# Optimization experiments

Hardware: AMD Instinct MI355X
Metric: run time of the kernel (lower is better)

Reference implementation:

```python
import jax, jax.numpy as jnp
import numpy as np

WS = 8      # window size
SS = 4      # shift size
NH = 4      # num heads
EPS = 1e-5
MLP_RATIO = 4


def _win_part(x, ws):
    # x: [B,D,H,W,C] -> [B*nD*nH*nW, ws^3, C]
    B, D, H, W, C = x.shape
    x = x.reshape(B, D // ws, ws, H // ws, ws, W // ws, ws, C)
    x = x.transpose(0, 1, 3, 5, 2, 4, 6, 7)
    return x.reshape(-1, ws * ws * ws, C)


def _win_rev(w, ws, B, D, H, W):
    C = w.shape[-1]
    x = w.reshape(B, D // ws, H // ws, W // ws, ws, ws, ws, C)
    x = x.transpose(0, 1, 4, 2, 5, 3, 6, 7)
    return x.reshape(B, D, H, W, C)


def _ln(x, g, b):
    m = jnp.mean(x, axis=-1, keepdims=True)
    v = jnp.mean((x - m) ** 2, axis=-1, keepdims=True)
    return (x - m) / jnp.sqrt(v + EPS) * g + b


def _rel_index(ws):
    coords = np.stack(np.meshgrid(np.arange(ws), np.arange(ws), np.arange(ws), indexing='ij'))  # [3,ws,ws,ws]
    cf = coords.reshape(3, -1)                      # [3, ws^3]
    rel = (cf[:, :, None] - cf[:, None, :]).transpose(1, 2, 0) + (ws - 1)  # [N,N,3]
    return rel[..., 0] * (2 * ws - 1) ** 2 + rel[..., 1] * (2 * ws - 1) + rel[..., 2]


def _attn_mask(D, H, W, ws, ss):
    img = np.zeros((1, D, H, W, 1), dtype=np.float32)
    cnt = 0
    sl = (slice(0, -ws), slice(-ws, -ss), slice(-ss, None))
    for d in sl:
        for h in sl:
            for w in sl:
                img[:, d, h, w, :] = cnt
                cnt += 1
    mw = np.asarray(_win_part(jnp.asarray(img), ws))[..., 0]  # [nW, ws^3]
    diff = mw[:, None, :] - mw[:, :, None]
    return np.where(diff != 0, -100.0, 0.0).astype(np.float32)


def setup_inputs() -> dict:
    key = jax.random.key(0)
    ks = jax.random.split(key, 12)
    B, D, H, W, C = 1, 16, 64, 64, 128
    mh = MLP_RATIO * C
    s = 0.02
    return {
        'x': jax.random.normal(ks[0], (B, D, H, W, C), jnp.float32),
        'attn_mask': jnp.asarray(_attn_mask(D, H, W, WS, SS)),
        'rel_index': jnp.asarray(_rel_index(WS), jnp.int32),
        'rel_bias': jax.random.normal(ks[1], ((2 * WS - 1) ** 3, NH), jnp.float32) * s,
        'qkv_w': jax.random.normal(ks[2], (3 * C, C), jnp.float32) * s,
        'qkv_b': jnp.zeros((3 * C,), jnp.float32),
        'proj_w': jax.random.normal(ks[3], (C, C), jnp.float32) * s,
        'proj_b': jnp.zeros((C,), jnp.float32),
        'norm1_g': jnp.ones((C,), jnp.float32),
        'norm1_b': jnp.zeros((C,), jnp.float32),
        'norm2_g': jnp.ones((C,), jnp.float32),
        'norm2_b': jnp.zeros((C,), jnp.float32),
        'mlp_w1': jax.random.normal(ks[4], (mh, C), jnp.float32) * s,
        'mlp_b1': jnp.zeros((mh,), jnp.float32),
        'mlp_w2': jax.random.normal(ks[5], (C, mh), jnp.float32) * s,
        'mlp_b2': jnp.zeros((C,), jnp.float32),
    }


def reference(x, attn_mask, rel_index, rel_bias, qkv_w, qkv_b, proj_w, proj_b,
              norm1_g, norm1_b, norm2_g, norm2_b, mlp_w1, mlp_b1, mlp_w2, mlp_b2):
    B, D, H, W, C = x.shape
    ws, ss, nh = WS, SS, NH
    hd = C // nh
    scale = hd ** -0.5
    N = ws ** 3
    shortcut = x
    h = _ln(x, norm1_g, norm1_b)
    h = jnp.roll(h, (-ss, -ss, -ss), axis=(1, 2, 3))
    xw = _win_part(h, ws)                 # [B_, N, C]
    B_ = xw.shape[0]
    nW = attn_mask.shape[0]
    qkv = xw @ qkv_w.T + qkv_b            # [B_, N, 3C]
    qkv = qkv.reshape(B_, N, 3, nh, hd).transpose(2, 0, 3, 1, 4)  # [3,B_,h,N,hd]
    q, k, v = qkv[0] * scale, qkv[1], qkv[2]
    attn = jnp.einsum('bhnd,bhmd->bhnm', q, k)
    rpe = rel_bias[rel_index.reshape(-1)].reshape(N, N, nh).transpose(2, 0, 1)  # [h,N,N]
    attn = attn + rpe[None]
    attn = attn.reshape(B_ // nW, nW, nh, N, N) + attn_mask[None, :, None]
    attn = jax.nn.softmax(attn.reshape(B_, nh, N, N), axis=-1)
    out = jnp.einsum('bhnm,bhmd->bhnd', attn, v).transpose(0, 2, 1, 3).reshape(B_, N, C)
    out = out @ proj_w.T + proj_b
    out = _win_rev(out, ws, B, D, H, W)
    out = jnp.roll(out, (ss, ss, ss), axis=(1, 2, 3))
    x = shortcut + out
    h2 = _ln(x, norm2_g, norm2_b)
    h2 = jax.nn.gelu(h2 @ mlp_w1.T + mlp_b1, approximate=False)
    return x + h2 @ mlp_w2.T + mlp_b2
```

## Files before the change

kernel.cpp:

```cpp
#include <hip/hip_runtime.h>
#include <math.h>

typedef __bf16 bf16;
typedef __bf16 bf16x4 __attribute__((ext_vector_type(4)));
typedef __bf16 bf16x8 __attribute__((ext_vector_type(8)));
typedef float f32x4 __attribute__((ext_vector_type(4)));
typedef unsigned short u16;
typedef u16 u16x2 __attribute__((ext_vector_type(2)));

#define LOG2E 1.4426950408889634f

__device__ __forceinline__ float b2f(u16 b) {
  return (float)__builtin_bit_cast(bf16, b);
}

__global__ void sniff_k(const unsigned* __restrict__ xw_, int* __restrict__ flag) {
  int lane = threadIdx.x;
  int c = 0;
#pragma unroll
  for (int j = 0; j < 4; j++) {
    unsigned e = (xw_[lane * 4 + j] >> 7) & 0xFFu;
    c += (e >= 100u && e <= 140u) ? 1 : 0;
  }
#pragma unroll
  for (int d = 1; d < 64; d <<= 1) c += __shfl_xor(c, d);
  if (lane == 0) *flag = (c >= 150) ? 1 : 0;
}

__global__ __launch_bounds__(256) void canon_big_k(const void* __restrict__ src,
                                                   bf16* __restrict__ dst,
                                                   const int* __restrict__ flag) {
  int i = (blockIdx.x * 256 + threadIdx.x) * 8;
  if (*flag) {
    *(bf16x8*)&dst[i] = *(const bf16x8*)((const bf16*)src + i);
  } else {
    const float* s = (const float*)src + i;
    bf16x8 v;
#pragma unroll
    for (int j = 0; j < 8; j++) v[j] = (bf16)s[j];
    *(bf16x8*)&dst[i] = v;
  }
}

struct CanonArgs {
  const void* src[13];
  bf16* dst[13];
  int n[13];
};

__global__ __launch_bounds__(256) void canon_small_k(CanonArgs a,
                                                     const int* __restrict__ flag) {
  int ti = blockIdx.y;
  int i = blockIdx.x * 256 + threadIdx.x;
  if (i >= a.n[ti]) return;
  if (*flag)
    a.dst[ti][i] = ((const bf16*)a.src[ti])[i];
  else
    a.dst[ti][i] = (bf16)((const float*)a.src[ti])[i];
}

__global__ __launch_bounds__(256) void rpem_k(const int* __restrict__ ridx,
                                              const bf16* __restrict__ rbias,
                                              bf16* __restrict__ rpem) {
  int t = blockIdx.x * 256 + threadIdx.x;
  int m0 = (t & 127) * 4, q = (t >> 7) & 511, h = (t >> 16) & 3, ty = t >> 18;
  int qd = q >> 6, qh = (q >> 3) & 7, qw = q & 7;
  int4 ri = *(const int4*)&ridx[q * 512 + m0];
  const int rv[4] = {ri.x, ri.y, ri.z, ri.w};
  bf16x4 o;
#pragma unroll
  for (int j = 0; j < 4; j++) {
    int m = m0 + j;
    int md = m >> 6, mh = (m >> 3) & 7, mw = m & 7;
    bool diff = ((ty & 4) && ((qd < 4) != (md < 4))) ||
                ((ty & 2) && ((qh < 4) != (mh < 4))) ||
                ((ty & 1) && ((qw < 4) != (mw < 4)));
    float v = (float)rbias[rv[j] * 4 + h] * LOG2E;
    o[j] = (bf16)(v + (diff ? -144.2695041f : 0.f));
  }
  *(bf16x4*)&rpem[(size_t)t * 4] = o;
}

template <int ROLL>
__global__ __launch_bounds__(256) void ln_k(const bf16* __restrict__ x,
                                            const bf16* __restrict__ g,
                                            const bf16* __restrict__ bsh,
                                            bf16* __restrict__ out) {
  int wave = threadIdx.x >> 6, lane = threadIdx.x & 63;
  int tok = blockIdx.x * 4 + wave;
  size_t src;
  if (ROLL) {
    int win = tok >> 9, pos = tok & 511;
    int rd = (win >> 6) * 8 + (pos >> 6);
    int rh = ((win >> 3) & 7) * 8 + ((pos >> 3) & 7);
    int rw = (win & 7) * 8 + (pos & 7);
    int od = (rd + 4) & 15, oh = (rh + 4) & 63, ow = (rw + 4) & 63;
    src = (size_t)((od * 64 + oh) * 64 + ow) * 128;
  } else {
    src = (size_t)tok * 128;
  }
  int ch = lane * 2;
  u16x2 xv = *(const u16x2*)(x + src + ch);
  float f0 = b2f(xv[0]), f1 = b2f(xv[1]);
  float s = f0 + f1, sq = f0 * f0 + f1 * f1;
#pragma unroll
  for (int d = 1; d < 64; d <<= 1) {
    s += __shfl_xor(s, d);
    sq += __shfl_xor(sq, d);
  }
  float mean = s * (1.f / 128.f);
  float var = sq * (1.f / 128.f) - mean * mean;
  float rstd = rsqrtf(fmaxf(var, 0.f) + 1e-5f);
  u16x2 gv = *(const u16x2*)(g + ch), bv = *(const u16x2*)(bsh + ch);
  u16x2 ov;
  ov[0] = __builtin_bit_cast(u16, (bf16)((f0 - mean) * rstd * b2f(gv[0]) + b2f(bv[0])));
  ov[1] = __builtin_bit_cast(u16, (bf16)((f1 - mean) * rstd * b2f(gv[1]) + b2f(bv[1])));
  *(u16x2*)(out + (size_t)tok * 128 + ch) = ov;
}

template <int EPI, int BM, int N_, int K_>
__global__ __launch_bounds__(256) void gemm_k(const bf16* __restrict__ A,
                                              const bf16* __restrict__ B,
                                              const bf16* __restrict__ bias,
                                              void* __restrict__ outv,
                                              const bf16* __restrict__ resid,
                                              const int* __restrict__ flag) {
  __shared__ __align__(16) u16 As[BM * 72];
  __shared__ __align__(16) u16 Bs[128 * 72];
  const int t = threadIdx.x;
  const int wave = t >> 6, lane = t & 63, l15 = lane & 15, quad = lane >> 4;
  const int m0 = blockIdx.x * BM, n0 = blockIdx.y * 128;
  constexpr int MI = BM / 32;
  constexpr int PA = BM / 32;
  int fl = 0;
  if constexpr (EPI == 3) fl = *flag;
  f32x4 acc[MI][4] = {};
  const int wr = (wave >> 1) * (BM / 2), wc = (wave & 1) * 64;
  const int srow = t >> 3, scol = (t & 7) * 8;
  constexpr int NC = K_ / 64;
  bf16x8 avA[PA], avB[PA];
#pragma unroll
  for (int p = 0; p < PA; p++) {
    int row = p * 32 + srow;
    avA[p] = *(const bf16x8*)(A + (size_t)(m0 + row) * K_ + scol);
  }
#pragma unroll
  for (int c = 0; c < NC; c++) {
    const bf16x8* av = (c & 1) ? avB : avA;
    bf16x8* avN = (c & 1) ? avA : avB;
    if (c + 1 < NC) {
#pragma unroll
      for (int p = 0; p < PA; p++) {
        int row = p * 32 + srow;
        avN[p] = *(const bf16x8*)(A + (size_t)(m0 + row) * K_ + (c + 1) * 64 + scol);
      }
    }
    bf16x8 bv[4];
#pragma unroll
    for (int p = 0; p < 4; p++) {
      int row = p * 32 + srow;
      bv[p] = *(const bf16x8*)(B + (size_t)(n0 + row) * K_ + c * 64 + scol);
    }
    __syncthreads();
#pragma unroll
    for (int p = 0; p < PA; p++)
      *(bf16x8*)&As[(p * 32 + srow) * 72 + scol] = av[p];
#pragma unroll
    for (int p = 0; p < 4; p++)
      *(bf16x8*)&Bs[(p * 32 + srow) * 72 + scol] = bv[p];
    __syncthreads();
#pragma unroll
    for (int ks = 0; ks < 2; ks++) {
      bf16x8 a[MI], b[4];
#pragma unroll
      for (int i = 0; i < MI; i++)
        a[i] = *(const bf16x8*)&As[(wr + i * 16 + l15) * 72 + ks * 32 + quad * 8];
#pragma unroll
      for (int j = 0; j < 4; j++)
        b[j] = *(const bf16x8*)&Bs[(wc + j * 16 + l15) * 72 + ks * 32 + quad * 8];
#pragma unroll
      for (int i = 0; i < MI; i++)
#pragma unroll
        for (int j = 0; j < 4; j++)
          acc[i][j] =
              __builtin_amdgcn_mfma_f32_16x16x32_bf16(a[i], b[j], acc[i][j], 0, 0, 0);
    }
  }
  const float qscale = 0.17677669529663687f * LOG2E;
#pragma unroll
  for (int i = 0; i < MI; i++) {
#pragma unroll
    for (int r = 0; r < 4; r++) {
      int tok = m0 + wr + i * 16 + quad * 4 + r;
      size_t obase = 0;
      if constexpr (EPI == 1) {
        int win = tok >> 9, pos = tok & 511;
        int rd = (win >> 6) * 8 + (pos >> 6);
        int rh = ((win >> 3) & 7) * 8 + ((pos >> 3) & 7);
        int rw = (win & 7) * 8 + (pos & 7);
        int od = (rd + 4) & 15, oh = (rh + 4) & 63, ow = (rw + 4) & 63;
        obase = (size_t)((od * 64 + oh) * 64 + ow) * 128;
      } else if constexpr (EPI != 0) {
        obase = (size_t)tok * N_;
      }
#pragma unroll
      for (int j = 0; j < 4; j++) {
        int gn = n0 + wc + j * 16 + l15;
        float v = acc[i][j][r] + (float)bias[gn];
        if constexpr (EPI == 0) {
          int tensor = gn >> 7, c = gn & 127, head = c >> 5, d = c & 31;
          if (tensor == 0) v *= qscale;
          int win = tok >> 9, pos = tok & 511;
          size_t off = ((((size_t)tensor * 4 + head) * 128 + win) * 512 + pos) * 32 + d;
          ((bf16*)outv)[off] = (bf16)v;
        } else if constexpr (EPI == 1) {
          v += (float)resid[obase + gn];
          ((bf16*)outv)[obase + gn] = (bf16)v;
        } else if constexpr (EPI == 2) {
          float v2 = v * v;
          float u2 = v * (2.30220806f + 0.10294323f * v2);
          float e2 = exp2f(u2);
          float rcp = __builtin_amdgcn_rcpf(e2 + 1.f);
          v = v - v * rcp;
          ((bf16*)outv)[obase + gn] = (bf16)v;
        } else {
          v += (float)resid[obase + gn];
          if (fl)
            ((bf16*)outv)[obase + gn] = (bf16)v;
          else
            ((float*)outv)[obase + gn] = v;
        }
      }
    }
  }
}

__global__ __launch_bounds__(512) void attn_k(const bf16* __restrict__ qkv,
                                              const bf16* __restrict__ rpem,
                                              bf16* __restrict__ att) {
  __shared__ __align__(16) bf16 sVt[32 * 512];
  __shared__ __align__(16) bf16 sP[8][32 * 64];
  const int t = threadIdx.x;
  const int p = blockIdx.x;
  const int win = ((p >> 6) << 3) | (p & 7);
  const int mid = (p >> 3) & 7;
  const int head = mid >> 1, qh = mid & 1;
  const int wave = t >> 6, lane = t & 63, l15 = lane & 15, quad = lane >> 4;

  const int wd = win >> 6, wh = (win >> 3) & 7, ww = win & 7;
  const int type = ((wd == 1) << 2) | ((wh == 7) << 1) | (ww == 7);

  const size_t hw32 = (size_t)512 * 32;
  const bf16* qp = qkv + ((size_t)(0 * 4 + head) * 128 + win) * hw32;
  const bf16* kp = qkv + ((size_t)(1 * 4 + head) * 128 + win) * hw32;
  const bf16* vp = qkv + ((size_t)(2 * 4 + head) * 128 + win) * hw32;
  const bf16* rpeh = rpem + (size_t)(type * 4 + head) * 512 * 512;
  const int qbase = qh * 256 + wave * 32;

  {
    int kpi = t >> 3, dblk = (t & 7) * 4;
    char* sb = (char*)sVt;
#pragma unroll
    for (int kb = 0; kb < 4; kb++) {
      const bf16* v0 = vp + (size_t)(kb * 128 + 2 * kpi) * 32 + dblk;
      bf16x4 a = *(const bf16x4*)v0;
      bf16x4 b = *(const bf16x4*)(v0 + 32);
      int keyw = kb * 64 + kpi;
#pragma unroll
      for (int dd = 0; dd < 4; dd++) {
        int row = dblk + dd;
        unsigned wv = (unsigned)__builtin_bit_cast(u16, a[dd]) |
                      ((unsigned)__builtin_bit_cast(u16, b[dd]) << 16);
        *(unsigned*)(sb + ((row * 1024 + keyw * 4) ^ ((row & 7) << 4))) = wv;
      }
    }
  }

  bf16x8 qa[2];
#pragma unroll
  for (int nt = 0; nt < 2; nt++)
    qa[nt] = *(const bf16x8*)(qp + (size_t)(qbase + nt * 16 + l15) * 32 + quad * 8);

  bf16x8 kb[4];
  bf16x4 rv[4][2];
#pragma unroll
  for (int mt = 0; mt < 4; mt++) {
    kb[mt] = *(const bf16x8*)(kp + (size_t)(mt * 16 + l15) * 32 + quad * 8);
#pragma unroll
    for (int nt = 0; nt < 2; nt++)
      rv[mt][nt] = *(const bf16x4*)(rpeh + (size_t)(qbase + nt * 16 + l15) * 512 +
                                    mt * 16 + quad * 4);
  }

  __syncthreads();

  f32x4 O[2][2] = {};
  float ls[2] = {0.f, 0.f};
  char* pw = (char*)sP[wave];
  const char* sv = (const char*)sVt;
  const int swz = (l15 & 7) << 4;

#pragma unroll
  for (int kt = 0; kt < 8; kt++) {
    bf16x8 kbn[4];
    bf16x4 rvn[4][2];
    if (kt < 7) {
#pragma unroll
      for (int mt = 0; mt < 4; mt++) {
        kbn[mt] = *(const bf16x8*)(kp +
                                   (size_t)((kt + 1) * 64 + mt * 16 + l15) * 32 +
                                   quad * 8);
#pragma unroll
        for (int nt = 0; nt < 2; nt++)
          rvn[mt][nt] =
              *(const bf16x4*)(rpeh + (size_t)(qbase + nt * 16 + l15) * 512 +
                               (kt + 1) * 64 + mt * 16 + quad * 4);
      }
    }
    f32x4 S[4][2];
#pragma unroll
    for (int mt = 0; mt < 4; mt++)
#pragma unroll
      for (int nt = 0; nt < 2; nt++) {
        f32x4 c;
#pragma unroll
        for (int r = 0; r < 4; r++) c[r] = (float)rv[mt][nt][r];
        S[mt][nt] = __builtin_amdgcn_mfma_f32_16x16x32_bf16(kb[mt], qa[nt], c, 0, 0, 0);
      }
#pragma unroll
    for (int nt = 0; nt < 2; nt++)
#pragma unroll
      for (int mt = 0; mt < 4; mt++) {
        bf16x4 pv;
#pragma unroll
        for (int r = 0; r < 4; r++) {
          float pe = exp2f(S[mt][nt][r]);
          ls[nt] += pe;
          pv[r] = (bf16)pe;
        }
        *(bf16x4*)(pw + (((nt * 16 + l15) * 128 + mt * 32 + quad * 8) ^ swz)) = pv;
      }
#pragma unroll
    for (int s = 0; s < 2; s++) {
      int vc = kt * 128 + s * 64 + quad * 16;
      int pc = s * 64 + quad * 16;
      bf16x8 va0 = *(const bf16x8*)(sv + ((l15 * 1024 + vc) ^ swz));
      bf16x8 va1 = *(const bf16x8*)(sv + (((16 + l15) * 1024 + vc) ^ swz));
      bf16x8 pb0 = *(const bf16x8*)(pw + ((l15 * 128 + pc) ^ swz));
      bf16x8 pb1 = *(const bf16x8*)(pw + (((16 + l15) * 128 + pc) ^ swz));
      O[0][0] = __builtin_amdgcn_mfma_f32_16x16x32_bf16(va0, pb0, O[0][0], 0, 0, 0);
      O[0][1] = __builtin_amdgcn_mfma_f32_16x16x32_bf16(va0, pb1, O[0][1], 0, 0, 0);
      O[1][0] = __builtin_amdgcn_mfma_f32_16x16x32_bf16(va1, pb0, O[1][0], 0, 0, 0);
      O[1][1] = __builtin_amdgcn_mfma_f32_16x16x32_bf16(va1, pb1, O[1][1], 0, 0, 0);
    }
#pragma unroll
    for (int mt = 0; mt < 4; mt++) {
      kb[mt] = kbn[mt];
      rv[mt][0] = rvn[mt][0];
      rv[mt][1] = rvn[mt][1];
    }
  }
#pragma unroll
  for (int nt = 0; nt < 2; nt++) {
    float l = ls[nt];
    l += __shfl_xor(l, 16);
    l += __shfl_xor(l, 32);
    float inv = __builtin_amdgcn_rcpf(l);
    int q = qbase + nt * 16 + l15;
#pragma unroll
    for (int dm = 0; dm < 2; dm++) {
      bf16x4 o;
#pragma unroll
      for (int r = 0; r < 4; r++) o[r] = (bf16)(O[dm][nt][r] * inv);
      *(bf16x4*)(att + ((size_t)win * 512 + q) * 128 + head * 32 + dm * 16 +
                 quad * 4) = o;
    }
  }
}

extern "C" void kernel_launch(void* const* d_in, const int* in_sizes, int n_in,
                              void* d_out, int out_size, void* d_ws,
                              size_t ws_size, hipStream_t stream) {
  const int* rel_index = (const int*)d_in[2];
  char* w = (char*)d_ws;

  int* flag = (int*)w;
  bf16* rb_c = (bf16*)(w + (64ull << 10));
  bf16* qw_c = (bf16*)(w + (128ull << 10));
  bf16* pw_c = (bf16*)(w + (256ull << 10));
  bf16* w1_c = (bf16*)(w + (320ull << 10));
  bf16* w2_c = (bf16*)(w + (512ull << 10));
  bf16* qb_c = (bf16*)(w + (704ull << 10));
  bf16* pb_c = (bf16*)(w + (708ull << 10));
  bf16* g1_c = (bf16*)(w + (712ull << 10));
  bf16* b1n_c = (bf16*)(w + (716ull << 10));
  bf16* g2_c = (bf16*)(w + (720ull << 10));
  bf16* b2n_c = (bf16*)(w + (724ull << 10));
  bf16* mb1_c = (bf16*)(w + (728ull << 10));
  bf16* mb2_c = (bf16*)(w + (732ull << 10));
  bf16* x_c = (bf16*)(w + (1ull << 20));
  bf16* xw = (bf16*)(w + (17ull << 20));
  bf16* qkvb = (bf16*)(w + (33ull << 20));
  bf16* x2 = (bf16*)(w + (99ull << 20));
  bf16* rpem = x2;
  bf16* att = xw;
  bf16* h2 = xw;
  bf16* a1 = qkvb;

  sniff_k<<<1, 64, 0, stream>>>((const unsigned*)d_in[0], flag);
  canon_big_k<<<4096, 256, 0, stream>>>(d_in[0], x_c, flag);

  CanonArgs ca;
  const int srcidx[13] = {3, 4, 5, 6, 7, 8, 9, 10, 11, 12, 13, 14, 15};
  bf16* dsts[13] = {rb_c, qw_c, qb_c, pw_c, pb_c, g1_c, b1n_c,
                    g2_c, b2n_c, w1_c, mb1_c, w2_c, mb2_c};
  for (int i = 0; i < 13; i++) {
    ca.src[i] = d_in[srcidx[i]];
    ca.dst[i] = dsts[i];
    ca.n[i] = in_sizes[srcidx[i]];
  }
  canon_small_k<<<dim3(256, 13), 256, 0, stream>>>(ca, flag);

  rpem_k<<<8192, 256, 0, stream>>>(rel_index, rb_c, rpem);
  ln_k<1><<<16384, 256, 0, stream>>>(x_c, g1_c, b1n_c, xw);
  gemm_k<0, 128, 384, 128><<<dim3(512, 3), 256, 0, stream>>>(xw, qw_c, qb_c,
                                                             qkvb, nullptr, flag);
  attn_k<<<1024, 512, 0, stream>>>(qkvb, rpem, att);
  gemm_k<1, 64, 128, 128><<<dim3(1024, 1), 256, 0, stream>>>(att, pw_c, pb_c,
                                                             x2, x_c, flag);
  ln_k<0><<<16384, 256, 0, stream>>>(x2, g2_c, b2n_c, h2);
  gemm_k<2, 128, 512, 128><<<dim3(512, 4), 256, 0, stream>>>(h2, w1_c, mb1_c,
                                                             a1, nullptr, flag);
  gemm_k<3, 64, 128, 512><<<dim3(1024, 1), 256, 0, stream>>>(a1, w2_c, mb2_c,
                                                             d_out, x2, flag);
}
```

Baseline: 461.6 us.

## Stage GEMM epilogue through LDS for vectorized stores; restructure attention row-sum

The GEMM epilogue now writes biased and activated results into shared memory, then re-reads them row-wise so each thread issues 16-byte vectorized global stores and residual loads instead of scattered 2-byte accesses. The attention kernel drops its register double-buffering of K and bias, stops unrolling the key loop, and adds an occupancy hint (launch_bounds 512,4) to cut register pressure. It also computes the softmax denominator with an MFMA against a ones vector, replacing per-lane adds and shuffles. The cost is an extra LDS round trip and barriers in the GEMM, less load/compute overlap in attention, and extra MFMA work.

```diff
diff --git a/kernel.cpp b/kernel.cpp
--- a/kernel.cpp
+++ b/kernel.cpp
@@ -125,8 +125,9 @@
                                               void* __restrict__ outv,
                                               const bf16* __restrict__ resid,
                                               const int* __restrict__ flag) {
-  __shared__ __align__(16) u16 As[BM * 72];
-  __shared__ __align__(16) u16 Bs[128 * 72];
+  __shared__ __align__(16) u16 SMEM[BM * 72 + 128 * 72];
+  u16* As = SMEM;
+  u16* Bs = SMEM + BM * 72;
   const int t = threadIdx.x;
   const int wave = t >> 6, lane = t & 63, l15 = lane & 15, quad = lane >> 4;
   const int m0 = blockIdx.x * BM, n0 = blockIdx.y * 128;
@@ -186,58 +187,91 @@
               __builtin_amdgcn_mfma_f32_16x16x32_bf16(a[i], b[j], acc[i][j], 0, 0, 0);
     }
   }
+  __syncthreads();
+  u16* Cs = SMEM;
   const float qscale = 0.17677669529663687f * LOG2E;
 #pragma unroll
-  for (int i = 0; i < MI; i++) {
-#pragma unroll
-    for (int r = 0; r < 4; r++) {
-      int tok = m0 + wr + i * 16 + quad * 4 + r;
-      size_t obase = 0;
-      if constexpr (EPI == 1) {
-        int win = tok >> 9, pos = tok & 511;
-        int rd = (win >> 6) * 8 + (pos >> 6);
-        int rh = ((win >> 3) & 7) * 8 + ((pos >> 3) & 7);
-        int rw = (win & 7) * 8 + (pos & 7);
-        int od = (rd + 4) & 15, oh = (rh + 4) & 63, ow = (rw + 4) & 63;
-        obase = (size_t)((od * 64 + oh) * 64 + ow) * 128;
-      } else if constexpr (EPI != 0) {
-        obase = (size_t)tok * N_;
-      }
-#pragma unroll
-      for (int j = 0; j < 4; j++) {
-        int gn = n0 + wc + j * 16 + l15;
-        float v = acc[i][j][r] + (float)bias[gn];
+  for (int i = 0; i < MI; i++)
+#pragma unroll
+    for (int j = 0; j < 4; j++) {
+      int c = wc + j * 16 + l15;
+      float bj = (float)bias[n0 + c];
+#pragma unroll
+      for (int r = 0; r < 4; r++) {
+        float v = acc[i][j][r] + bj;
         if constexpr (EPI == 0) {
-          int tensor = gn >> 7, c = gn & 127, head = c >> 5, d = c & 31;
-          if (tensor == 0) v *= qscale;
-          int win = tok >> 9, pos = tok & 511;
-          size_t off = ((((size_t)tensor * 4 + head) * 128 + win) * 512 + pos) * 32 + d;
-          ((bf16*)outv)[off] = (bf16)v;
-        } else if constexpr (EPI == 1) {
-          v += (float)resid[obase + gn];
-          ((bf16*)outv)[obase + gn] = (bf16)v;
-        } else if constexpr (EPI == 2) {
+          if (n0 == 0) v *= qscale;
+        }
+        if constexpr (EPI == 2) {
           float v2 = v * v;
           float u2 = v * (2.30220806f + 0.10294323f * v2);
           float e2 = exp2f(u2);
           float rcp = __builtin_amdgcn_rcpf(e2 + 1.f);
           v = v - v * rcp;
-          ((bf16*)outv)[obase + gn] = (bf16)v;
-        } else {
-          v += (float)resid[obase + gn];
-          if (fl)
-            ((bf16*)outv)[obase + gn] = (bf16)v;
-          else
-            ((float*)outv)[obase + gn] = v;
         }
-      }
-    }
-  }
-}
-
-__global__ __launch_bounds__(512) void attn_k(const bf16* __restrict__ qkv,
-                                              const bf16* __restrict__ rpem,
-                                              bf16* __restrict__ att) {
+        Cs[(wr + i * 16 + quad * 4 + r) * 136 + c] =
+            __builtin_bit_cast(u16, (bf16)v);
+      }
+    }
+  __syncthreads();
+  constexpr int TPR = 256 / BM;
+  constexpr int CPT = 128 / TPR;
+  const int row = t / TPR, chb = (t % TPR) * CPT;
+  const int tok = m0 + row;
+  size_t obase = 0;
+  if constexpr (EPI == 1) {
+    int win = tok >> 9, pos = tok & 511;
+    int rd = (win >> 6) * 8 + (pos >> 6);
+    int rh = ((win >> 3) & 7) * 8 + ((pos >> 3) & 7);
+    int rw = (win & 7) * 8 + (pos & 7);
+    int od = (rd + 4) & 15, oh = (rh + 4) & 63, ow = (rw + 4) & 63;
+    obase = (size_t)((od * 64 + oh) * 64 + ow) * 128;
+  } else if constexpr (EPI == 2) {
+    obase = (size_t)tok * N_ + n0;
+  } else if constexpr (EPI == 3) {
+    obase = (size_t)tok * N_;
+  }
+#pragma unroll
+  for (int cc = 0; cc < CPT / 8; cc++) {
+    int c0 = chb + cc * 8;
+    bf16x8 cv = *(const bf16x8*)&Cs[row * 136 + c0];
+    if constexpr (EPI == 0) {
+      int win = tok >> 9, pos = tok & 511;
+      int tensor = n0 >> 7, head = c0 >> 5, d = c0 & 31;
+      size_t off =
+          ((((size_t)tensor * 4 + head) * 128 + win) * 512 + pos) * 32 + d;
+      *(bf16x8*)((bf16*)outv + off) = cv;
+    } else if constexpr (EPI == 1) {
+      bf16x8 rv8 = *(const bf16x8*)(resid + obase + c0);
+      bf16x8 o;
+#pragma unroll
+      for (int e = 0; e < 8; e++) o[e] = (bf16)((float)cv[e] + (float)rv8[e]);
+      *(bf16x8*)((bf16*)outv + obase + c0) = o;
+    } else if constexpr (EPI == 2) {
+      *(bf16x8*)((bf16*)outv + obase + c0) = cv;
+    } else {
+      bf16x8 rv8 = *(const bf16x8*)(resid + obase + c0);
+      float fo[8];
+#pragma unroll
+      for (int e = 0; e < 8; e++) fo[e] = (float)cv[e] + (float)rv8[e];
+      if (fl) {
+        bf16x8 o;
+#pragma unroll
+        for (int e = 0; e < 8; e++) o[e] = (bf16)fo[e];
+        *(bf16x8*)((bf16*)outv + obase + c0) = o;
+      } else {
+        f32x4 o0 = {fo[0], fo[1], fo[2], fo[3]};
+        f32x4 o1 = {fo[4], fo[5], fo[6], fo[7]};
+        *(f32x4*)((float*)outv + obase + c0) = o0;
+        *(f32x4*)((float*)outv + obase + c0 + 4) = o1;
+      }
+    }
+  }
+}
+
+__global__ __launch_bounds__(512, 4) void attn_k(const bf16* __restrict__ qkv,
+                                                 const bf16* __restrict__ rpem,
+                                                 bf16* __restrict__ att) {
   __shared__ __align__(16) bf16 sVt[32 * 512];
   __shared__ __align__(16) bf16 sP[8][32 * 64];
   const int t = threadIdx.x;
@@ -281,41 +315,31 @@
   for (int nt = 0; nt < 2; nt++)
     qa[nt] = *(const bf16x8*)(qp + (size_t)(qbase + nt * 16 + l15) * 32 + quad * 8);
 
-  bf16x8 kb[4];
-  bf16x4 rv[4][2];
-#pragma unroll
-  for (int mt = 0; mt < 4; mt++) {
-    kb[mt] = *(const bf16x8*)(kp + (size_t)(mt * 16 + l15) * 32 + quad * 8);
-#pragma unroll
-    for (int nt = 0; nt < 2; nt++)
-      rv[mt][nt] = *(const bf16x4*)(rpeh + (size_t)(qbase + nt * 16 + l15) * 512 +
-                                    mt * 16 + quad * 4);
-  }
+  bf16x8 ones;
+#pragma unroll
+  for (int e = 0; e < 8; e++) ones[e] = (bf16)1.0f;
 
   __syncthreads();
 
   f32x4 O[2][2] = {};
-  float ls[2] = {0.f, 0.f};
+  f32x4 O2[2] = {};
   char* pw = (char*)sP[wave];
   const char* sv = (const char*)sVt;
   const int swz = (l15 & 7) << 4;
 
-#pragma unroll
+#pragma unroll 1
   for (int kt = 0; kt < 8; kt++) {
-    bf16x8 kbn[4];
-    bf16x4 rvn[4][2];
-    if (kt < 7) {
-#pragma unroll
-      for (int mt = 0; mt < 4; mt++) {
-        kbn[mt] = *(const bf16x8*)(kp +
-                                   (size_t)((kt + 1) * 64 + mt * 16 + l15) * 32 +
-                                   quad * 8);
-#pragma unroll
-        for (int nt = 0; nt < 2; nt++)
-          rvn[mt][nt] =
-              *(const bf16x4*)(rpeh + (size_t)(qbase + nt * 16 + l15) * 512 +
-                               (kt + 1) * 64 + mt * 16 + quad * 4);
-      }
+    bf16x8 kb[4];
+    bf16x4 rv[4][2];
+#pragma unroll
+    for (int mt = 0; mt < 4; mt++) {
+      kb[mt] = *(const bf16x8*)(kp + (size_t)(kt * 64 + mt * 16 + l15) * 32 +
+                                quad * 8);
+#pragma unroll
+      for (int nt = 0; nt < 2; nt++)
+        rv[mt][nt] =
+            *(const bf16x4*)(rpeh + (size_t)(qbase + nt * 16 + l15) * 512 +
+                             kt * 64 + mt * 16 + quad * 4);
     }
     f32x4 S[4][2];
 #pragma unroll
@@ -333,11 +357,7 @@
       for (int mt = 0; mt < 4; mt++) {
         bf16x4 pv;
 #pragma unroll
-        for (int r = 0; r < 4; r++) {
-          float pe = exp2f(S[mt][nt][r]);
-          ls[nt] += pe;
-          pv[r] = (bf16)pe;
-        }
+        for (int r = 0; r < 4; r++) pv[r] = (bf16)exp2f(S[mt][nt][r]);
         *(bf16x4*)(pw + (((nt * 16 + l15) * 128 + mt * 32 + quad * 8) ^ swz)) = pv;
       }
 #pragma unroll
@@ -352,20 +372,13 @@
       O[0][1] = __builtin_amdgcn_mfma_f32_16x16x32_bf16(va0, pb1, O[0][1], 0, 0, 0);
       O[1][0] = __builtin_amdgcn_mfma_f32_16x16x32_bf16(va1, pb0, O[1][0], 0, 0, 0);
       O[1][1] = __builtin_amdgcn_mfma_f32_16x16x32_bf16(va1, pb1, O[1][1], 0, 0, 0);
-    }
-#pragma unroll
-    for (int mt = 0; mt < 4; mt++) {
-      kb[mt] = kbn[mt];
-      rv[mt][0] = rvn[mt][0];
-      rv[mt][1] = rvn[mt][1];
+      O2[0] = __builtin_amdgcn_mfma_f32_16x16x32_bf16(ones, pb0, O2[0], 0, 0, 0);
+      O2[1] = __builtin_amdgcn_mfma_f32_16x16x32_bf16(ones, pb1, O2[1], 0, 0, 0);
     }
   }
 #pragma unroll
   for (int nt = 0; nt < 2; nt++) {
-    float l = ls[nt];
-    l += __shfl_xor(l, 16);
-    l += __shfl_xor(l, 32);
-    float inv = __builtin_amdgcn_rcpf(l);
+    float inv = __builtin_amdgcn_rcpf(O2[nt][0]);
     int q = qbase + nt * 16 + l15;
 #pragma unroll
     for (int dm = 0; dm < 2; dm++) {
```

Result: faster. 437.5 us (-5.2%).

## Ping-pong K/RPE register tiles, compute row sums via MFMA, set occupancy bound

Applied to the files above, without the earlier changes.

The attention kernel now double-buffers the K and relative-position-bias register tiles in a non-unrolled loop that handles two tiles per iteration, where before it fully unrolled all eight tiles. It also drops the per-element scalar softmax denominator accumulation and shuffle reduction. The row sum is instead computed with extra MFMAs against a vector of ones, which sums the bf16-rounded probabilities. A launch bound of 4 waves-per-EU minimum is added to cap register use and raise occupancy. The cost is extra MFMA work, and the bound risks register spills.

```diff
diff --git a/kernel.cpp b/kernel.cpp
--- a/kernel.cpp
+++ b/kernel.cpp
@@ -235,9 +235,9 @@
   }
 }
 
-__global__ __launch_bounds__(512) void attn_k(const bf16* __restrict__ qkv,
-                                              const bf16* __restrict__ rpem,
-                                              bf16* __restrict__ att) {
+__global__ __launch_bounds__(512, 4) void attn_k(const bf16* __restrict__ qkv,
+                                                 const bf16* __restrict__ rpem,
+                                                 bf16* __restrict__ att) {
   __shared__ __align__(16) bf16 sVt[32 * 512];
   __shared__ __align__(16) bf16 sP[8][32 * 64];
   const int t = threadIdx.x;
@@ -281,42 +281,32 @@
   for (int nt = 0; nt < 2; nt++)
     qa[nt] = *(const bf16x8*)(qp + (size_t)(qbase + nt * 16 + l15) * 32 + quad * 8);
 
-  bf16x8 kb[4];
-  bf16x4 rv[4][2];
-#pragma unroll
-  for (int mt = 0; mt < 4; mt++) {
-    kb[mt] = *(const bf16x8*)(kp + (size_t)(mt * 16 + l15) * 32 + quad * 8);
-#pragma unroll
-    for (int nt = 0; nt < 2; nt++)
-      rv[mt][nt] = *(const bf16x4*)(rpeh + (size_t)(qbase + nt * 16 + l15) * 512 +
-                                    mt * 16 + quad * 4);
-  }
+  bf16x8 ones;
+#pragma unroll
+  for (int e = 0; e < 8; e++) ones[e] = (bf16)1.0f;
 
   __syncthreads();
 
   f32x4 O[2][2] = {};
-  float ls[2] = {0.f, 0.f};
+  f32x4 O2[2] = {};
   char* pw = (char*)sP[wave];
   const char* sv = (const char*)sVt;
   const int swz = (l15 & 7) << 4;
 
-#pragma unroll
-  for (int kt = 0; kt < 8; kt++) {
-    bf16x8 kbn[4];
-    bf16x4 rvn[4][2];
-    if (kt < 7) {
-#pragma unroll
-      for (int mt = 0; mt < 4; mt++) {
-        kbn[mt] = *(const bf16x8*)(kp +
-                                   (size_t)((kt + 1) * 64 + mt * 16 + l15) * 32 +
-                                   quad * 8);
-#pragma unroll
-        for (int nt = 0; nt < 2; nt++)
-          rvn[mt][nt] =
-              *(const bf16x4*)(rpeh + (size_t)(qbase + nt * 16 + l15) * 512 +
-                               (kt + 1) * 64 + mt * 16 + quad * 4);
-      }
-    }
+  auto load_tile = [&](int kt, bf16x8 (&kbv)[4], bf16x4 (&rvv)[4][2]) {
+#pragma unroll
+    for (int mt = 0; mt < 4; mt++) {
+      kbv[mt] = *(const bf16x8*)(kp + (size_t)(kt * 64 + mt * 16 + l15) * 32 +
+                                 quad * 8);
+#pragma unroll
+      for (int nt = 0; nt < 2; nt++)
+        rvv[mt][nt] =
+            *(const bf16x4*)(rpeh + (size_t)(qbase + nt * 16 + l15) * 512 +
+                             kt * 64 + mt * 16 + quad * 4);
+    }
+  };
+
+  auto compute_tile = [&](int kt, bf16x8 (&kbv)[4], bf16x4 (&rvv)[4][2]) {
     f32x4 S[4][2];
 #pragma unroll
     for (int mt = 0; mt < 4; mt++)
@@ -324,8 +314,9 @@
       for (int nt = 0; nt < 2; nt++) {
         f32x4 c;
 #pragma unroll
-        for (int r = 0; r < 4; r++) c[r] = (float)rv[mt][nt][r];
-        S[mt][nt] = __builtin_amdgcn_mfma_f32_16x16x32_bf16(kb[mt], qa[nt], c, 0, 0, 0);
+        for (int r = 0; r < 4; r++) c[r] = (float)rvv[mt][nt][r];
+        S[mt][nt] =
+            __builtin_amdgcn_mfma_f32_16x16x32_bf16(kbv[mt], qa[nt], c, 0, 0, 0);
       }
 #pragma unroll
     for (int nt = 0; nt < 2; nt++)
@@ -333,11 +324,7 @@
       for (int mt = 0; mt < 4; mt++) {
         bf16x4 pv;
 #pragma unroll
-        for (int r = 0; r < 4; r++) {
-          float pe = exp2f(S[mt][nt][r]);
-          ls[nt] += pe;
-          pv[r] = (bf16)pe;
-        }
+        for (int r = 0; r < 4; r++) pv[r] = (bf16)exp2f(S[mt][nt][r]);
         *(bf16x4*)(pw + (((nt * 16 + l15) * 128 + mt * 32 + quad * 8) ^ swz)) = pv;
       }
 #pragma unroll
@@ -352,20 +339,25 @@
       O[0][1] = __builtin_amdgcn_mfma_f32_16x16x32_bf16(va0, pb1, O[0][1], 0, 0, 0);
       O[1][0] = __builtin_amdgcn_mfma_f32_16x16x32_bf16(va1, pb0, O[1][0], 0, 0, 0);
       O[1][1] = __builtin_amdgcn_mfma_f32_16x16x32_bf16(va1, pb1, O[1][1], 0, 0, 0);
-    }
-#pragma unroll
-    for (int mt = 0; mt < 4; mt++) {
-      kb[mt] = kbn[mt];
-      rv[mt][0] = rvn[mt][0];
-      rv[mt][1] = rvn[mt][1];
-    }
+      O2[0] = __builtin_amdgcn_mfma_f32_16x16x32_bf16(ones, pb0, O2[0], 0, 0, 0);
+      O2[1] = __builtin_amdgcn_mfma_f32_16x16x32_bf16(ones, pb1, O2[1], 0, 0, 0);
+    }
+  };
+
+  bf16x8 kbA[4], kbB[4];
+  bf16x4 rvA[4][2], rvB[4][2];
+  load_tile(0, kbA, rvA);
+#pragma unroll 1
+  for (int i = 0; i < 4; i++) {
+    int kt = 2 * i;
+    load_tile(kt + 1, kbB, rvB);
+    compute_tile(kt, kbA, rvA);
+    if (kt + 2 < 8) load_tile(kt + 2, kbA, rvA);
+    compute_tile(kt + 1, kbB, rvB);
   }
 #pragma unroll
   for (int nt = 0; nt < 2; nt++) {
-    float l = ls[nt];
-    l += __shfl_xor(l, 16);
-    l += __shfl_xor(l, 32);
-    float inv = __builtin_amdgcn_rcpf(l);
+    float inv = __builtin_amdgcn_rcpf(O2[nt][0]);
     int q = qbase + nt * 16 + l15;
 #pragma unroll
     for (int dm = 0; dm < 2; dm++) {
```

New measurement: 422.1 us. 1.09x faster.
